# Optimization experiments

Hardware: AMD Instinct MI355X
Metric: run time of the kernel (lower is better)

The kernel has to match this reference:

```python
import jax, jax.numpy as jnp
import numpy as np

B, T, D, H, F = 4, 2048, 1024, 16, 4096
HD = D // H
EPS = 1e-5


def setup_inputs() -> dict:
    key = jax.random.key(0)
    ks = jax.random.split(key, 10)
    s = lambda fan_in: 1.0 / np.sqrt(fan_in)
    return {
        "x": jax.random.normal(ks[0], (B, T, D), jnp.float32),
        "ln1_g": jnp.ones((D,), jnp.float32),
        "ln1_b": jnp.zeros((D,), jnp.float32),
        "ln2_g": jnp.ones((D,), jnp.float32),
        "ln2_b": jnp.zeros((D,), jnp.float32),
        "Wq": jax.random.normal(ks[1], (H, D, HD), jnp.float32) * s(D),
        "Wk": jax.random.normal(ks[2], (H, D, HD), jnp.float32) * s(D),
        "Wv": jax.random.normal(ks[3], (H, D, HD), jnp.float32) * s(D),
        "Wo": jax.random.normal(ks[4], (D, D), jnp.float32) * s(D),
        "bo": jnp.zeros((D,), jnp.float32),
        "W1": jax.random.normal(ks[5], (D, F), jnp.float32) * s(D),
        "b1": jnp.zeros((F,), jnp.float32),
        "W2": jax.random.normal(ks[6], (F, D), jnp.float32) * s(F),
        "b2": jnp.zeros((D,), jnp.float32),
    }


def _layernorm(x, g, b):
    mu = jnp.mean(x, axis=-1, keepdims=True)
    var = jnp.mean(jnp.square(x - mu), axis=-1, keepdims=True)
    return (x - mu) * jax.lax.rsqrt(var + EPS) * g + b


def reference(x, ln1_g, ln1_b, ln2_g, ln2_b, Wq, Wk, Wv, Wo, bo, W1, b1, W2, b2):
    Bc, Tc, Dc = x.shape
    xn = _layernorm(x, ln1_g, ln1_b)
    # per-head projections (source loops over heads; here batched over h)
    q = jnp.einsum('btd,hdk->bhtk', xn, Wq)
    k = jnp.einsum('btd,hdk->bhtk', xn, Wk)
    v = jnp.einsum('btd,hdk->bhtk', xn, Wv)
    scale = jnp.asarray(Dc, x.dtype) ** -0.5  # C**-0.5 with C = embedding_dim
    scores = jnp.einsum('bhtk,bhsk->bhts', q, k) * scale
    causal = jnp.tril(jnp.ones((Tc, Tc), bool))
    scores = jnp.where(causal, scores, -jnp.inf)
    attn = jax.nn.softmax(scores, axis=-1)
    out = jnp.einsum('bhts,bhsk->bhtk', attn, v)
    out = out.transpose(0, 2, 1, 3).reshape(Bc, Tc, Dc)  # concat heads
    attn_out = out @ Wo + bo
    h = attn_out + x  # residual 1
    hn = _layernorm(h, ln2_g, ln2_b)
    ff = jax.nn.relu(hn @ W1 + b1) @ W2 + b2
    return ff + h  # residual 2
```

## Files before the change

### kernel.cpp

```cpp
#include <hip/hip_runtime.h>
#include <hip/hip_bf16.h>

#define NB 4
#define NT 2048
#define ND 1024
#define NH 16
#define NHD 64
#define NF 4096
#define MTOK (NB*NT)

typedef float f32x4 __attribute__((ext_vector_type(4)));
typedef __bf16 bf16x8 __attribute__((ext_vector_type(8)));
typedef short s16x8 __attribute__((ext_vector_type(8)));
typedef unsigned short ushort_t;

__device__ inline ushort_t f2bf(float f) {
    unsigned int u = __builtin_bit_cast(unsigned int, f);
    unsigned int r = (u + 0x7FFFu + ((u >> 16) & 1u)) >> 16;
    return (ushort_t)r;
}

__device__ __forceinline__ void async_load16(const void* g, void* l) {
    __builtin_amdgcn_global_load_lds(
        (const __attribute__((address_space(1))) void*)g,
        (__attribute__((address_space(3))) void*)l, 16, 0, 0);
}

__device__ __forceinline__ unsigned int cvt_pk_bf16(float lo, float hi) {
    unsigned int r;
    asm("v_cvt_pk_bf16_f32 %0, %1, %2" : "=v"(r) : "v"(lo), "v"(hi));
    return r;
}

__device__ __forceinline__ float exp2_fast(float x) {
    float r;
    asm("v_exp_f32 %0, %1" : "=v"(r) : "v"(x));
    return r;
}

__global__ __launch_bounds__(256)
void transpose_to_bf16(const float* __restrict__ src, ushort_t* __restrict__ dst,
                       int R, int C) {
    __shared__ float tile[32][33];
    int c0 = blockIdx.x * 32, r0 = blockIdx.y * 32;
    #pragma unroll
    for (int i = 0; i < 32; i += 8)
        tile[threadIdx.y + i][threadIdx.x] =
            src[(size_t)(r0 + threadIdx.y + i) * C + c0 + threadIdx.x];
    __syncthreads();
    #pragma unroll
    for (int i = 0; i < 32; i += 8)
        dst[(size_t)(c0 + threadIdx.y + i) * R + r0 + threadIdx.x] =
            f2bf(tile[threadIdx.x][threadIdx.y + i]);
}

__global__ __launch_bounds__(256)
void transpose_qkv_to_bf16(const float* __restrict__ Wq, const float* __restrict__ Wk,
                           const float* __restrict__ Wv, ushort_t* __restrict__ dst) {
    __shared__ float tile[32][33];
    int z = blockIdx.z;
    int w = z >> 4, h = z & 15;
    const float* src = (w == 0 ? Wq : (w == 1 ? Wk : Wv)) + (size_t)h * ND * NHD;
    const float sc = (w == 0) ? 0.03125f * 1.44269504f : 1.0f;
    ushort_t* out = dst + ((size_t)w * ND + h * NHD) * ND;
    int c0 = blockIdx.x * 32, r0 = blockIdx.y * 32;
    #pragma unroll
    for (int i = 0; i < 32; i += 8)
        tile[threadIdx.y + i][threadIdx.x] =
            src[(size_t)(r0 + threadIdx.y + i) * NHD + c0 + threadIdx.x];
    __syncthreads();
    #pragma unroll
    for (int i = 0; i < 32; i += 8)
        out[(size_t)(c0 + threadIdx.y + i) * ND + r0 + threadIdx.x] =
            f2bf(tile[threadIdx.x][threadIdx.y + i] * sc);
}

__global__ __launch_bounds__(256)
void layernorm_to_bf16(const float* __restrict__ x, const float* __restrict__ g,
                       const float* __restrict__ bvec, ushort_t* __restrict__ out) {
    int row = blockIdx.x;
    const float4* xr = (const float4*)(x + (size_t)row * ND);
    float4 v = xr[threadIdx.x];
    float s = v.x + v.y + v.z + v.w;
    float s2 = v.x * v.x + v.y * v.y + v.z * v.z + v.w * v.w;
    #pragma unroll
    for (int o = 32; o >= 1; o >>= 1) {
        s += __shfl_xor(s, o);
        s2 += __shfl_xor(s2, o);
    }
    __shared__ float red[8];
    int wave = threadIdx.x >> 6, lane = threadIdx.x & 63;
    if (lane == 0) { red[wave] = s; red[4 + wave] = s2; }
    __syncthreads();
    float ts = red[0] + red[1] + red[2] + red[3];
    float ts2 = red[4] + red[5] + red[6] + red[7];
    float mu = ts * (1.f / ND);
    float var = ts2 * (1.f / ND) - mu * mu;
    float rs = rsqrtf(var + 1e-5f);
    float4 gv = ((const float4*)g)[threadIdx.x];
    float4 bv = ((const float4*)bvec)[threadIdx.x];
    ushort4 o4;
    o4.x = f2bf((v.x - mu) * rs * gv.x + bv.x);
    o4.y = f2bf((v.y - mu) * rs * gv.y + bv.y);
    o4.z = f2bf((v.z - mu) * rs * gv.z + bv.z);
    o4.w = f2bf((v.w - mu) * rs * gv.w + bv.w);
    ((ushort4*)(out + (size_t)row * ND))[threadIdx.x] = o4;
}

template<int BN, bool HAS_BIAS, bool RELU, bool HAS_RES, bool OUT_F32>
__global__ __launch_bounds__(512, 2)
void gemm256(const ushort_t* __restrict__ A, const ushort_t* __restrict__ Bt,
             const float* __restrict__ bias, const float* __restrict__ res,
             void* __restrict__ outp, int M, int N, int K) {
    constexpr int NFR = BN / 64;
    constexpr int BISS = BN / 64;
    __shared__ __align__(16) ushort_t As[2][256 * 64];
    __shared__ __align__(16) ushort_t Bs[2][BN * 64];
    const int t = threadIdx.x;
    const int wave = t >> 6, lane = t & 63;
    const int wm = wave >> 2, wn = wave & 3;
    const int g = lane >> 4, l16 = lane & 15;
    int wid = blockIdx.y * gridDim.x + blockIdx.x;
    const int cpx = (gridDim.x * gridDim.y) >> 3;
    wid = (wid & 7) * cpx + (wid >> 3);
    const int m0 = (wid / gridDim.x) * 256;
    const int n0 = (wid % gridDim.x) * BN;
    const int lrow8 = lane >> 3;
    const int srcCol = ((lane & 7) ^ lrow8) * 8;
    const ushort_t* Abase = A + (size_t)m0 * K + srcCol;
    const ushort_t* Bbase = Bt + (size_t)n0 * K + srcCol;
    const int NKT = K >> 6;

    f32x4 acc[8][NFR] = {};

    auto stageA = [&](int kt, int slot) {
        #pragma unroll
        for (int j = 0; j < 4; j++) {
            const int rowbase = j * 64 + wave * 8;
            async_load16(Abase + (size_t)(rowbase + lrow8) * K + kt * 64,
                         &As[slot][rowbase * 64]);
        }
    };
    auto stageB = [&](int kt, int slot) {
        #pragma unroll
        for (int j = 0; j < BISS; j++) {
            const int rowbase = j * 64 + wave * 8;
            async_load16(Bbase + (size_t)(rowbase + lrow8) * K + kt * 64,
                         &Bs[slot][rowbase * 64]);
        }
    };

    stageA(0, 0);
    stageB(0, 0);
    stageB(1, 1);

    for (int kt = 0; kt < NKT; ++kt) {
        const int cur = kt & 1;
        if (kt == NKT - 1) {
            asm volatile("s_waitcnt vmcnt(0)" ::: "memory");
        } else if constexpr (BN == 256) {
            asm volatile("s_waitcnt vmcnt(4)" ::: "memory");
        } else {
            asm volatile("s_waitcnt vmcnt(2)" ::: "memory");
        }
        __builtin_amdgcn_s_barrier();

        const ushort_t* as = As[cur];
        const ushort_t* bs = Bs[cur];

        bf16x8 bfr[NFR][2];
        #pragma unroll
        for (int nf = 0; nf < NFR; nf++)
            #pragma unroll
            for (int ks = 0; ks < 2; ks++) {
                const int row = wn * (BN / 4) + nf * 16 + l16;
                int a = row * 128 + ks * 64 + 16 * g;
                a ^= (row & 7) << 4;
                bfr[nf][ks] = *(const bf16x8*)((const char*)bs + a);
            }
        if (kt + 1 < NKT) stageA(kt + 1, cur ^ 1);

        #pragma unroll
        for (int q = 0; q < 4; q++) {
            if (q == 2) {
                __builtin_amdgcn_s_barrier();
                if (kt + 2 < NKT) stageB(kt + 2, cur);
            }
            bf16x8 af[2][2];
            #pragma unroll
            for (int mi2 = 0; mi2 < 2; mi2++)
                #pragma unroll
                for (int ks = 0; ks < 2; ks++) {
                    const int row = wm * 128 + (q * 2 + mi2) * 16 + l16;
                    int a = row * 128 + ks * 64 + 16 * g;
                    a ^= (row & 7) << 4;
                    af[mi2][ks] = *(const bf16x8*)((const char*)as + a);
                }
            __builtin_amdgcn_s_setprio(1);
            #pragma unroll
            for (int mi2 = 0; mi2 < 2; mi2++)
                #pragma unroll
                for (int nf = 0; nf < NFR; nf++)
                    #pragma unroll
                    for (int ks = 0; ks < 2; ks++)
                        acc[q * 2 + mi2][nf] = __builtin_amdgcn_mfma_f32_16x16x32_bf16(
                            af[mi2][ks], bfr[nf][ks], acc[q * 2 + mi2][nf], 0, 0, 0);
            __builtin_amdgcn_s_setprio(0);
        }
    }

    const int gr0 = m0 + wm * 128 + g * 4;
    const int gc0 = n0 + wn * (BN / 4) + l16;
    #pragma unroll
    for (int mi = 0; mi < 8; mi++) {
        #pragma unroll
        for (int nf = 0; nf < NFR; nf++) {
            const int col = gc0 + nf * 16;
            float bb = 0.f;
            if constexpr (HAS_BIAS) bb = bias[col];
            #pragma unroll
            for (int r = 0; r < 4; r++) {
                const int row = gr0 + mi * 16 + r;
                float v = acc[mi][nf][r] + bb;
                if constexpr (RELU) v = fmaxf(v, 0.f);
                if constexpr (HAS_RES) v += res[(size_t)row * N + col];
                if constexpr (OUT_F32)
                    ((float*)outp)[(size_t)row * N + col] = v;
                else
                    ((ushort_t*)outp)[(size_t)row * N + col] = f2bf(v);
            }
        }
    }
}

__global__ __launch_bounds__(256)
void attn_kernel(const ushort_t* __restrict__ qkv, ushort_t* __restrict__ out) {
    __shared__ __align__(16) ushort_t Ks[64 * 64];
    __shared__ __align__(16) ushort_t Vt[64 * 64];
    __shared__ unsigned int Pw[4][32][35];
    const int L = blockIdx.y * gridDim.x + blockIdx.x;
    const int xcd = L & 7, kk = L >> 3;
    const int bh = ((kk & 7) << 3) | xcd;
    const int pairIdx = kk >> 3;
    const int b = bh >> 4, h = bh & 15;
    const int t = threadIdx.x, wave = t >> 6, lane = t & 63;
    const int g = lane >> 4, q16 = lane & 15;
    const size_t base = ((size_t)b * NT) * 3072 + h * NHD;
    const ushort_t* qp_base = qkv + base;
    const ushort_t* kb = qkv + base + 1024;
    const ushort_t* vb = qkv + base + 2048;
    const int krw = lane >> 3, kck = lane & 7;
    const int ksrc = (kck ^ krw) * 8;
    const int vkp = t >> 3, vdg = t & 7;

    for (int half = 0; half < 2; half++) {
        const int qt = half ? (15 - pairIdx) : pairIdx;
        const int q0 = qt * 128;
        const int wq0 = q0 + wave * 32;
        bf16x8 qf[2][2];
        #pragma unroll
        for (int qb2 = 0; qb2 < 2; qb2++) {
            const ushort_t* qp = qp_base + (size_t)(wq0 + 16 * qb2 + q16) * 3072 + 8 * g;
            qf[qb2][0] = *(const bf16x8*)qp;
            qf[qb2][1] = *(const bf16x8*)(qp + 32);
        }
        f32x4 of[2][4] = {};
        float m_run[2] = {-1.0e30f, -1.0e30f};
        float l_run[2] = {0.f, 0.f};
        const int nkv = 2 * qt + 2;

        for (int kv = 0; kv < nkv; ++kv) {
            __syncthreads();
            #pragma unroll
            for (int c = 0; c < 2; c++) {
                const int rowbase = c * 32 + wave * 8;
                async_load16(kb + (size_t)(kv * 64 + rowbase + krw) * 3072 + ksrc,
                             Ks + rowbase * 64);
            }
            {
                const ushort_t* vp = vb + (size_t)(kv * 64 + 2 * vkp) * 3072 + vdg * 8;
                s16x8 v0 = *(const s16x8*)vp;
                s16x8 v1 = *(const s16x8*)(vp + 3072);
                #pragma unroll
                for (int dd = 0; dd < 8; dd++) {
                    int d = vdg * 8 + dd;
                    unsigned int wv = (unsigned int)(ushort_t)v0[dd] |
                                      ((unsigned int)(ushort_t)v1[dd] << 16);
                    int a = (d << 7) + (vkp << 2);
                    a ^= (((d & 7) ^ ((d >> 3) & 7)) << 4);
                    *(unsigned int*)((char*)Vt + a) = wv;
                }
            }
            __syncthreads();

            const int kbase = kv * 64;
            if (kbase > wq0 + 31) continue;

            bf16x8 kf[4][2];
            #pragma unroll
            for (int n = 0; n < 4; n++)
                #pragma unroll
                for (int kd = 0; kd < 2; kd++) {
                    int row = n * 16 + q16;
                    int a = row * 128 + (kd * 64 + 16 * g);
                    a ^= ((row & 7) << 4);
                    kf[n][kd] = *(const bf16x8*)((const char*)Ks + a);
                }

            f32x4 sf[2][4] = {};
            #pragma unroll
            for (int n = 0; n < 4; n++)
                #pragma unroll
                for (int kd = 0; kd < 2; kd++) {
                    sf[0][n] = __builtin_amdgcn_mfma_f32_16x16x32_bf16(
                        kf[n][kd], qf[0][kd], sf[0][n], 0, 0, 0);
                    sf[1][n] = __builtin_amdgcn_mfma_f32_16x16x32_bf16(
                        kf[n][kd], qf[1][kd], sf[1][n], 0, 0, 0);
                }

            #pragma unroll
            for (int qb2 = 0; qb2 < 2; qb2++) {
                const int wqb = wq0 + 16 * qb2 + q16;
                const bool partial = (kbase + 63 > wq0 + 16 * qb2);
                float p[4][4];
                #pragma unroll
                for (int n = 0; n < 4; n++)
                    #pragma unroll
                    for (int r = 0; r < 4; r++) {
                        float v = sf[qb2][n][r];
                        if (partial) {
                            int kg = kbase + n * 16 + 4 * g + r;
                            if (kg > wqb) v = -1.0e30f;
                        }
                        p[n][r] = v;
                    }
                float mx0 = fmaxf(fmaxf(p[0][0], p[0][1]), fmaxf(p[0][2], p[0][3]));
                float mx1 = fmaxf(fmaxf(p[1][0], p[1][1]), fmaxf(p[1][2], p[1][3]));
                float mx2 = fmaxf(fmaxf(p[2][0], p[2][1]), fmaxf(p[2][2], p[2][3]));
                float mx3 = fmaxf(fmaxf(p[3][0], p[3][1]), fmaxf(p[3][2], p[3][3]));
                float mx = fmaxf(fmaxf(mx0, mx1), fmaxf(mx2, mx3));
                mx = fmaxf(mx, __shfl_xor(mx, 16));
                mx = fmaxf(mx, __shfl_xor(mx, 32));
                if (__any(mx > m_run[qb2] + 11.5f)) {
                    float mn = fmaxf(m_run[qb2], mx);
                    float corr = exp2_fast(m_run[qb2] - mn);
                    m_run[qb2] = mn;
                    l_run[qb2] *= corr;
                    #pragma unroll
                    for (int nf = 0; nf < 4; nf++) {
                        f32x4 o4 = of[qb2][nf];
                        o4[0] *= corr; o4[1] *= corr; o4[2] *= corr; o4[3] *= corr;
                        of[qb2][nf] = o4;
                    }
                }
                float ps = 0.f;
                #pragma unroll
                for (int n = 0; n < 4; n++)
                    #pragma unroll
                    for (int r = 0; r < 4; r++) {
                        p[n][r] = exp2_fast(p[n][r] - m_run[qb2]);
                        ps += p[n][r];
                    }
                ps += __shfl_xor(ps, 16);
                ps += __shfl_xor(ps, 32);
                l_run[qb2] += ps;
                unsigned int* pr = &Pw[wave][16 * qb2 + q16][0];
                #pragma unroll
                for (int n = 0; n < 4; n++) {
                    pr[8 * n + 2 * g + 0] = cvt_pk_bf16(p[n][0], p[n][1]);
                    pr[8 * n + 2 * g + 1] = cvt_pk_bf16(p[n][2], p[n][3]);
                }
            }

            #pragma unroll
            for (int kbk = 0; kbk < 2; kbk++) {
                bf16x8 pfr[2];
                #pragma unroll
                for (int qb2 = 0; qb2 < 2; qb2++) {
                    const unsigned int* pr = &Pw[wave][16 * qb2 + q16][0];
                    uint4 pu;
                    pu.x = pr[16 * kbk + 4 * g + 0];
                    pu.y = pr[16 * kbk + 4 * g + 1];
                    pu.z = pr[16 * kbk + 4 * g + 2];
                    pu.w = pr[16 * kbk + 4 * g + 3];
                    pfr[qb2] = __builtin_bit_cast(bf16x8, pu);
                }
                #pragma unroll
                for (int nf = 0; nf < 4; nf++) {
                    const int d = nf * 16 + q16;
                    int a = (d << 7) + (kbk * 64 + 16 * g);
                    a ^= (((d & 7) ^ ((d >> 3) & 7)) << 4);
                    bf16x8 vf = *(const bf16x8*)((const char*)Vt + a);
                    of[0][nf] = __builtin_amdgcn_mfma_f32_16x16x32_bf16(
                        vf, pfr[0], of[0][nf], 0, 0, 0);
                    of[1][nf] = __builtin_amdgcn_mfma_f32_16x16x32_bf16(
                        vf, pfr[1], of[1][nf], 0, 0, 0);
                }
            }
        }

        #pragma unroll
        for (int qb2 = 0; qb2 < 2; qb2++) {
            float rl = 1.f / l_run[qb2];
            const size_t orow = (size_t)b * NT + q0 + wave * 32 + 16 * qb2 + q16;
            #pragma unroll
            for (int nf = 0; nf < 4; nf++) {
                ushort4 o4;
                o4.x = f2bf(of[qb2][nf][0] * rl);
                o4.y = f2bf(of[qb2][nf][1] * rl);
                o4.z = f2bf(of[qb2][nf][2] * rl);
                o4.w = f2bf(of[qb2][nf][3] * rl);
                *(ushort4*)(out + orow * ND + h * NHD + nf * 16 + 4 * g) = o4;
            }
        }
    }
}

extern "C" void kernel_launch(void* const* d_in, const int* in_sizes, int n_in,
                              void* d_out, int out_size, void* d_ws, size_t ws_size,
                              hipStream_t stream) {
    const float* x     = (const float*)d_in[0];
    const float* ln1_g = (const float*)d_in[1];
    const float* ln1_b = (const float*)d_in[2];
    const float* ln2_g = (const float*)d_in[3];
    const float* ln2_b = (const float*)d_in[4];
    const float* Wq    = (const float*)d_in[5];
    const float* Wk    = (const float*)d_in[6];
    const float* Wv    = (const float*)d_in[7];
    const float* Wo    = (const float*)d_in[8];
    const float* bo    = (const float*)d_in[9];
    const float* W1    = (const float*)d_in[10];
    const float* b1    = (const float*)d_in[11];
    const float* W2    = (const float*)d_in[12];
    const float* b2    = (const float*)d_in[13];
    float* outp = (float*)d_out;

    char* w = (char*)d_ws;
    ushort_t* Wqkv_t = (ushort_t*)(w);
    ushort_t* Wo_t   = (ushort_t*)(w + 6291456);
    ushort_t* W1_t   = (ushort_t*)(w + 8388608);
    ushort_t* W2_t   = (ushort_t*)(w + 16777216);
    ushort_t* xn     = (ushort_t*)(w + 25165824);
    ushort_t* qkv    = (ushort_t*)(w + 41943040);
    ushort_t* attn_o = qkv + (size_t)MTOK * 3072;
    ushort_t* ff1    = qkv;
    float*    hbuf   = (float*)(w + 41943040 + 67108864);

    dim3 tb(32, 8);
    transpose_qkv_to_bf16<<<dim3(2, 32, 48), tb, 0, stream>>>(Wq, Wk, Wv, Wqkv_t);
    transpose_to_bf16<<<dim3(32, 32), tb, 0, stream>>>(Wo, Wo_t, 1024, 1024);
    transpose_to_bf16<<<dim3(128, 32), tb, 0, stream>>>(W1, W1_t, 1024, 4096);
    transpose_to_bf16<<<dim3(32, 128), tb, 0, stream>>>(W2, W2_t, 4096, 1024);

    layernorm_to_bf16<<<MTOK, 256, 0, stream>>>(x, ln1_g, ln1_b, xn);

    gemm256<128, false, false, false, false><<<dim3(24, 32), 512, 0, stream>>>(
        xn, Wqkv_t, nullptr, nullptr, qkv, MTOK, 3072, 1024);

    attn_kernel<<<dim3(8, 64), 256, 0, stream>>>(qkv, attn_o);

    gemm256<128, true, false, true, true><<<dim3(8, 32), 512, 0, stream>>>(
        attn_o, Wo_t, bo, x, hbuf, MTOK, 1024, 1024);

    layernorm_to_bf16<<<MTOK, 256, 0, stream>>>(hbuf, ln2_g, ln2_b, xn);

    gemm256<256, true, true, false, false><<<dim3(16, 32), 512, 0, stream>>>(
        xn, W1_t, b1, nullptr, ff1, MTOK, NF, 1024);

    gemm256<128, true, false, true, true><<<dim3(8, 32), 512, 0, stream>>>(
        ff1, W2_t, b2, hbuf, outp, MTOK, 1024, NF);
}
```

Before: 388.9 us.

## Restructure GEMM into 8-phase half-tile load pipeline with per-phase barriers

Rewrites the bf16 GEMM main loop so that A and B tile loads are issued in halves spread across four compute phases per k-step. Each phase has its own vmcnt wait and barriers, and the wave-to-row mapping of A fragments is interleaved so every phase reads a 64-row slice written by one half-load. The aim is to overlap global-to-LDS traffic with MFMA work more evenly and avoid one large wait at the top of each iteration. In exchange it adds more barriers per iteration and relies on tight vmcnt accounting, where a mistake would cause races.

```diff
diff --git a/kernel.cpp b/kernel.cpp
--- a/kernel.cpp
+++ b/kernel.cpp
@@ -109,11 +109,10 @@
 
 template<int BN, bool HAS_BIAS, bool RELU, bool HAS_RES, bool OUT_F32>
 __global__ __launch_bounds__(512, 2)
-void gemm256(const ushort_t* __restrict__ A, const ushort_t* __restrict__ Bt,
-             const float* __restrict__ bias, const float* __restrict__ res,
-             void* __restrict__ outp, int M, int N, int K) {
+void gemm8p(const ushort_t* __restrict__ A, const ushort_t* __restrict__ Bt,
+            const float* __restrict__ bias, const float* __restrict__ res,
+            void* __restrict__ outp, int M, int N, int K) {
     constexpr int NFR = BN / 64;
-    constexpr int BISS = BN / 64;
     __shared__ __align__(16) ushort_t As[2][256 * 64];
     __shared__ __align__(16) ushort_t Bs[2][BN * 64];
     const int t = threadIdx.x;
@@ -133,69 +132,79 @@
 
     f32x4 acc[8][NFR] = {};
 
-    auto stageA = [&](int kt, int slot) {
+    auto stageAhalf = [&](int kt, int h, int slot) {
         #pragma unroll
-        for (int j = 0; j < 4; j++) {
+        for (int j = 2 * h; j < 2 * h + 2; j++) {
             const int rowbase = j * 64 + wave * 8;
             async_load16(Abase + (size_t)(rowbase + lrow8) * K + kt * 64,
                          &As[slot][rowbase * 64]);
         }
     };
-    auto stageB = [&](int kt, int slot) {
-        #pragma unroll
-        for (int j = 0; j < BISS; j++) {
-            const int rowbase = j * 64 + wave * 8;
+    auto stageBhalf = [&](int kt, int h, int slot) {
+        if constexpr (BN == 256) {
+            #pragma unroll
+            for (int j = 2 * h; j < 2 * h + 2; j++) {
+                const int rowbase = j * 64 + wave * 8;
+                async_load16(Bbase + (size_t)(rowbase + lrow8) * K + kt * 64,
+                             &Bs[slot][rowbase * 64]);
+            }
+        } else {
+            const int rowbase = h * 64 + wave * 8;
             async_load16(Bbase + (size_t)(rowbase + lrow8) * K + kt * 64,
                          &Bs[slot][rowbase * 64]);
         }
     };
 
-    stageA(0, 0);
-    stageB(0, 0);
-    stageB(1, 1);
+    stageAhalf(0, 0, 0); stageAhalf(0, 1, 0);
+    stageBhalf(0, 0, 0); stageBhalf(0, 1, 0);
+    stageBhalf(1, 0, 1); stageBhalf(1, 1, 1);
+    stageAhalf(1, 0, 1);
+    if constexpr (BN == 256) asm volatile("s_waitcnt vmcnt(6)" ::: "memory");
+    else                     asm volatile("s_waitcnt vmcnt(4)" ::: "memory");
+    __builtin_amdgcn_s_barrier();
+    __builtin_amdgcn_sched_barrier(0);
 
     for (int kt = 0; kt < NKT; ++kt) {
-        const int cur = kt & 1;
-        if (kt == NKT - 1) {
-            asm volatile("s_waitcnt vmcnt(0)" ::: "memory");
-        } else if constexpr (BN == 256) {
-            asm volatile("s_waitcnt vmcnt(4)" ::: "memory");
-        } else {
-            asm volatile("s_waitcnt vmcnt(2)" ::: "memory");
-        }
-        __builtin_amdgcn_s_barrier();
-
+        const int cur = kt & 1, nxt = cur ^ 1;
         const ushort_t* as = As[cur];
         const ushort_t* bs = Bs[cur];
-
         bf16x8 bfr[NFR][2];
         #pragma unroll
-        for (int nf = 0; nf < NFR; nf++)
-            #pragma unroll
-            for (int ks = 0; ks < 2; ks++) {
-                const int row = wn * (BN / 4) + nf * 16 + l16;
-                int a = row * 128 + ks * 64 + 16 * g;
-                a ^= (row & 7) << 4;
-                bfr[nf][ks] = *(const bf16x8*)((const char*)bs + a);
-            }
-        if (kt + 1 < NKT) stageA(kt + 1, cur ^ 1);
-
-        #pragma unroll
         for (int q = 0; q < 4; q++) {
-            if (q == 2) {
-                __builtin_amdgcn_s_barrier();
-                if (kt + 2 < NKT) stageB(kt + 2, cur);
+            if (q == 0) {
+                #pragma unroll
+                for (int nf = 0; nf < NFR; nf++)
+                    #pragma unroll
+                    for (int ks = 0; ks < 2; ks++) {
+                        const int row = wn * (BN / 4) + nf * 16 + l16;
+                        int a = row * 128 + ks * 64 + 16 * g;
+                        a ^= (row & 7) << 4;
+                        bfr[nf][ks] = *(const bf16x8*)((const char*)bs + a);
+                    }
             }
             bf16x8 af[2][2];
             #pragma unroll
             for (int mi2 = 0; mi2 < 2; mi2++)
                 #pragma unroll
                 for (int ks = 0; ks < 2; ks++) {
-                    const int row = wm * 128 + (q * 2 + mi2) * 16 + l16;
+                    const int row = q * 64 + wm * 32 + mi2 * 16 + l16;
                     int a = row * 128 + ks * 64 + 16 * g;
                     a ^= (row & 7) << 4;
                     af[mi2][ks] = *(const bf16x8*)((const char*)as + a);
                 }
+            if (q == 0)      { if (kt + 1 < NKT) stageAhalf(kt + 1, 1, nxt); }
+            else if (q == 1) { if (kt + 2 < NKT) stageBhalf(kt + 2, 0, cur); }
+            else if (q == 2) { if (kt + 2 < NKT) stageBhalf(kt + 2, 1, cur); }
+            else             { if (kt + 2 < NKT) stageAhalf(kt + 2, 0, cur); }
+            __builtin_amdgcn_sched_barrier(0);
+            if (kt < NKT - 2) {
+                if constexpr (BN == 256) asm volatile("s_waitcnt vmcnt(8)" ::: "memory");
+                else                     asm volatile("s_waitcnt vmcnt(6)" ::: "memory");
+            } else {
+                asm volatile("s_waitcnt vmcnt(0)" ::: "memory");
+            }
+            __builtin_amdgcn_s_barrier();
+            __builtin_amdgcn_sched_barrier(0);
             __builtin_amdgcn_s_setprio(1);
             #pragma unroll
             for (int mi2 = 0; mi2 < 2; mi2++)
@@ -206,13 +215,15 @@
                         acc[q * 2 + mi2][nf] = __builtin_amdgcn_mfma_f32_16x16x32_bf16(
                             af[mi2][ks], bfr[nf][ks], acc[q * 2 + mi2][nf], 0, 0, 0);
             __builtin_amdgcn_s_setprio(0);
+            __builtin_amdgcn_s_barrier();
+            __builtin_amdgcn_sched_barrier(0);
         }
     }
 
-    const int gr0 = m0 + wm * 128 + g * 4;
     const int gc0 = n0 + wn * (BN / 4) + l16;
     #pragma unroll
     for (int mi = 0; mi < 8; mi++) {
+        const int rowb = m0 + (mi >> 1) * 64 + wm * 32 + (mi & 1) * 16 + g * 4;
         #pragma unroll
         for (int nf = 0; nf < NFR; nf++) {
             const int col = gc0 + nf * 16;
@@ -220,7 +231,7 @@
             if constexpr (HAS_BIAS) bb = bias[col];
             #pragma unroll
             for (int r = 0; r < 4; r++) {
-                const int row = gr0 + mi * 16 + r;
+                const int row = rowb + r;
                 float v = acc[mi][nf][r] + bb;
                 if constexpr (RELU) v = fmaxf(v, 0.f);
                 if constexpr (HAS_RES) v += res[(size_t)row * N + col];
@@ -454,19 +465,19 @@
 
     layernorm_to_bf16<<<MTOK, 256, 0, stream>>>(x, ln1_g, ln1_b, xn);
 
-    gemm256<128, false, false, false, false><<<dim3(24, 32), 512, 0, stream>>>(
+    gemm8p<128, false, false, false, false><<<dim3(24, 32), 512, 0, stream>>>(
         xn, Wqkv_t, nullptr, nullptr, qkv, MTOK, 3072, 1024);
 
     attn_kernel<<<dim3(8, 64), 256, 0, stream>>>(qkv, attn_o);
 
-    gemm256<128, true, false, true, true><<<dim3(8, 32), 512, 0, stream>>>(
+    gemm8p<128, true, false, true, true><<<dim3(8, 32), 512, 0, stream>>>(
         attn_o, Wo_t, bo, x, hbuf, MTOK, 1024, 1024);
 
     layernorm_to_bf16<<<MTOK, 256, 0, stream>>>(hbuf, ln2_g, ln2_b, xn);
 
-    gemm256<256, true, true, false, false><<<dim3(16, 32), 512, 0, stream>>>(
+    gemm8p<256, true, true, false, false><<<dim3(16, 32), 512, 0, stream>>>(
         xn, W1_t, b1, nullptr, ff1, MTOK, NF, 1024);
 
-    gemm256<128, true, false, true, true><<<dim3(8, 32), 512, 0, stream>>>(
+    gemm8p<128, true, false, true, true><<<dim3(8, 32), 512, 0, stream>>>(
         ff1, W2_t, b2, hbuf, outp, MTOK, 1024, NF);
 }
```

Result: slower. 396.8 us (+2.0%).

## Double-buffer K/V tiles in attention kernel to overlap loads with compute

Applied to the files above, without the earlier changes.

The attention kernel now keeps two LDS buffers each for K and transposed V. It issues the global loads for the next KV tile before computing on the current one, then writes V into the other buffer after compute, leaving one barrier per iteration. This is meant to hide global-load latency behind the MFMA and softmax work. It doubles K/V LDS use, which may lower occupancy, and raises register pressure because the prefetched V values are held across the compute.

```diff
diff --git a/kernel.cpp b/kernel.cpp
--- a/kernel.cpp
+++ b/kernel.cpp
@@ -235,8 +235,8 @@
 
 __global__ __launch_bounds__(256)
 void attn_kernel(const ushort_t* __restrict__ qkv, ushort_t* __restrict__ out) {
-    __shared__ __align__(16) ushort_t Ks[64 * 64];
-    __shared__ __align__(16) ushort_t Vt[64 * 64];
+    __shared__ __align__(16) ushort_t Ks[2][64 * 64];
+    __shared__ __align__(16) ushort_t Vt[2][64 * 64];
     __shared__ unsigned int Pw[4][32][35];
     const int L = blockIdx.y * gridDim.x + blockIdx.x;
     const int xcd = L & 7, kk = L >> 3;
@@ -253,6 +253,31 @@
     const int ksrc = (kck ^ krw) * 8;
     const int vkp = t >> 3, vdg = t & 7;
 
+    auto stageK = [&](int kv, int buf) {
+        #pragma unroll
+        for (int c = 0; c < 2; c++) {
+            const int rowbase = c * 32 + wave * 8;
+            async_load16(kb + (size_t)(kv * 64 + rowbase + krw) * 3072 + ksrc,
+                         &Ks[buf][rowbase * 64]);
+        }
+    };
+    auto loadV = [&](int kv, s16x8& v0, s16x8& v1) {
+        const ushort_t* vp = vb + (size_t)(kv * 64 + 2 * vkp) * 3072 + vdg * 8;
+        v0 = *(const s16x8*)vp;
+        v1 = *(const s16x8*)(vp + 3072);
+    };
+    auto writeV = [&](int buf, const s16x8& v0, const s16x8& v1) {
+        #pragma unroll
+        for (int dd = 0; dd < 8; dd++) {
+            int d = vdg * 8 + dd;
+            unsigned int wv = (unsigned int)(ushort_t)v0[dd] |
+                              ((unsigned int)(ushort_t)v1[dd] << 16);
+            int a = (d << 7) + (vkp << 2);
+            a ^= (((d & 7) ^ ((d >> 3) & 7)) << 4);
+            *(unsigned int*)((char*)&Vt[buf][0] + a) = wv;
+        }
+    };
+
     for (int half = 0; half < 2; half++) {
         const int qt = half ? (15 - pairIdx) : pairIdx;
         const int q0 = qt * 128;
@@ -269,134 +294,132 @@
         float l_run[2] = {0.f, 0.f};
         const int nkv = 2 * qt + 2;
 
+        {
+            s16x8 pv0, pv1;
+            stageK(0, 0);
+            loadV(0, pv0, pv1);
+            asm volatile("s_waitcnt vmcnt(0)" ::: "memory");
+            writeV(0, pv0, pv1);
+        }
+        __syncthreads();
+
         for (int kv = 0; kv < nkv; ++kv) {
+            const int cur = kv & 1, nxt = cur ^ 1;
+            s16x8 pv0, pv1;
+            const bool pre = (kv + 1 < nkv);
+            if (pre) {
+                stageK(kv + 1, nxt);
+                loadV(kv + 1, pv0, pv1);
+            }
+            __builtin_amdgcn_sched_barrier(0);
+
+            const int kbase = kv * 64;
+            if (kbase <= wq0 + 31) {
+                bf16x8 kf[4][2];
+                #pragma unroll
+                for (int n = 0; n < 4; n++)
+                    #pragma unroll
+                    for (int kd = 0; kd < 2; kd++) {
+                        int row = n * 16 + q16;
+                        int a = row * 128 + (kd * 64 + 16 * g);
+                        a ^= ((row & 7) << 4);
+                        kf[n][kd] = *(const bf16x8*)((const char*)&Ks[cur][0] + a);
+                    }
+
+                f32x4 sf[2][4] = {};
+                #pragma unroll
+                for (int n = 0; n < 4; n++)
+                    #pragma unroll
+                    for (int kd = 0; kd < 2; kd++) {
+                        sf[0][n] = __builtin_amdgcn_mfma_f32_16x16x32_bf16(
+                            kf[n][kd], qf[0][kd], sf[0][n], 0, 0, 0);
+                        sf[1][n] = __builtin_amdgcn_mfma_f32_16x16x32_bf16(
+                            kf[n][kd], qf[1][kd], sf[1][n], 0, 0, 0);
+                    }
+
+                #pragma unroll
+                for (int qb2 = 0; qb2 < 2; qb2++) {
+                    const int wqb = wq0 + 16 * qb2 + q16;
+                    const bool partial = (kbase + 63 > wq0 + 16 * qb2);
+                    float p[4][4];
+                    #pragma unroll
+                    for (int n = 0; n < 4; n++)
+                        #pragma unroll
+                        for (int r = 0; r < 4; r++) {
+                            float v = sf[qb2][n][r];
+                            if (partial) {
+                                int kg = kbase + n * 16 + 4 * g + r;
+                                if (kg > wqb) v = -1.0e30f;
+                            }
+                            p[n][r] = v;
+                        }
+                    float mx0 = fmaxf(fmaxf(p[0][0], p[0][1]), fmaxf(p[0][2], p[0][3]));
+                    float mx1 = fmaxf(fmaxf(p[1][0], p[1][1]), fmaxf(p[1][2], p[1][3]));
+                    float mx2 = fmaxf(fmaxf(p[2][0], p[2][1]), fmaxf(p[2][2], p[2][3]));
+                    float mx3 = fmaxf(fmaxf(p[3][0], p[3][1]), fmaxf(p[3][2], p[3][3]));
+                    float mx = fmaxf(fmaxf(mx0, mx1), fmaxf(mx2, mx3));
+                    mx = fmaxf(mx, __shfl_xor(mx, 16));
+                    mx = fmaxf(mx, __shfl_xor(mx, 32));
+                    if (__any(mx > m_run[qb2] + 11.5f)) {
+                        float mn = fmaxf(m_run[qb2], mx);
+                        float corr = exp2_fast(m_run[qb2] - mn);
+                        m_run[qb2] = mn;
+                        l_run[qb2] *= corr;
+                        #pragma unroll
+                        for (int nf = 0; nf < 4; nf++) {
+                            f32x4 o4 = of[qb2][nf];
+                            o4[0] *= corr; o4[1] *= corr; o4[2] *= corr; o4[3] *= corr;
+                            of[qb2][nf] = o4;
+                        }
+                    }
+                    float ps = 0.f;
+                    #pragma unroll
+                    for (int n = 0; n < 4; n++)
+                        #pragma unroll
+                        for (int r = 0; r < 4; r++) {
+                            p[n][r] = exp2_fast(p[n][r] - m_run[qb2]);
+                            ps += p[n][r];
+                        }
+                    ps += __shfl_xor(ps, 16);
+                    ps += __shfl_xor(ps, 32);
+                    l_run[qb2] += ps;
+                    unsigned int* pr = &Pw[wave][16 * qb2 + q16][0];
+                    #pragma unroll
+                    for (int n = 0; n < 4; n++) {
+                        pr[8 * n + 2 * g + 0] = cvt_pk_bf16(p[n][0], p[n][1]);
+                        pr[8 * n + 2 * g + 1] = cvt_pk_bf16(p[n][2], p[n][3]);
+                    }
+                }
+
+                #pragma unroll
+                for (int kbk = 0; kbk < 2; kbk++) {
+                    bf16x8 pfr[2];
+                    #pragma unroll
+                    for (int qb2 = 0; qb2 < 2; qb2++) {
+                        const unsigned int* pr = &Pw[wave][16 * qb2 + q16][0];
+                        uint4 pu;
+                        pu.x = pr[16 * kbk + 4 * g + 0];
+                        pu.y = pr[16 * kbk + 4 * g + 1];
+                        pu.z = pr[16 * kbk + 4 * g + 2];
+                        pu.w = pr[16 * kbk + 4 * g + 3];
+                        pfr[qb2] = __builtin_bit_cast(bf16x8, pu);
+                    }
+                    #pragma unroll
+                    for (int nf = 0; nf < 4; nf++) {
+                        const int d = nf * 16 + q16;
+                        int a = (d << 7) + (kbk * 64 + 16 * g);
+                        a ^= (((d & 7) ^ ((d >> 3) & 7)) << 4);
+                        bf16x8 vf = *(const bf16x8*)((const char*)&Vt[cur][0] + a);
+                        of[0][nf] = __builtin_amdgcn_mfma_f32_16x16x32_bf16(
+                            vf, pfr[0], of[0][nf], 0, 0, 0);
+                        of[1][nf] = __builtin_amdgcn_mfma_f32_16x16x32_bf16(
+                            vf, pfr[1], of[1][nf], 0, 0, 0);
+                    }
+                }
+            }
+
+            if (pre) writeV(nxt, pv0, pv1);
             __syncthreads();
-            #pragma unroll
-            for (int c = 0; c < 2; c++) {
-                const int rowbase = c * 32 + wave * 8;
-                async_load16(kb + (size_t)(kv * 64 + rowbase + krw) * 3072 + ksrc,
-                             Ks + rowbase * 64);
-            }
-            {
-                const ushort_t* vp = vb + (size_t)(kv * 64 + 2 * vkp) * 3072 + vdg * 8;
-                s16x8 v0 = *(const s16x8*)vp;
-                s16x8 v1 = *(const s16x8*)(vp + 3072);
-                #pragma unroll
-                for (int dd = 0; dd < 8; dd++) {
-                    int d = vdg * 8 + dd;
-                    unsigned int wv = (unsigned int)(ushort_t)v0[dd] |
-                                      ((unsigned int)(ushort_t)v1[dd] << 16);
-                    int a = (d << 7) + (vkp << 2);
-                    a ^= (((d & 7) ^ ((d >> 3) & 7)) << 4);
-                    *(unsigned int*)((char*)Vt + a) = wv;
-                }
-            }
-            __syncthreads();
-
-            const int kbase = kv * 64;
-            if (kbase > wq0 + 31) continue;
-
-            bf16x8 kf[4][2];
-            #pragma unroll
-            for (int n = 0; n < 4; n++)
-                #pragma unroll
-                for (int kd = 0; kd < 2; kd++) {
-                    int row = n * 16 + q16;
-                    int a = row * 128 + (kd * 64 + 16 * g);
-                    a ^= ((row & 7) << 4);
-                    kf[n][kd] = *(const bf16x8*)((const char*)Ks + a);
-                }
-
-            f32x4 sf[2][4] = {};
-            #pragma unroll
-            for (int n = 0; n < 4; n++)
-                #pragma unroll
-                for (int kd = 0; kd < 2; kd++) {
-                    sf[0][n] = __builtin_amdgcn_mfma_f32_16x16x32_bf16(
-                        kf[n][kd], qf[0][kd], sf[0][n], 0, 0, 0);
-                    sf[1][n] = __builtin_amdgcn_mfma_f32_16x16x32_bf16(
-                        kf[n][kd], qf[1][kd], sf[1][n], 0, 0, 0);
-                }
-
-            #pragma unroll
-            for (int qb2 = 0; qb2 < 2; qb2++) {
-                const int wqb = wq0 + 16 * qb2 + q16;
-                const bool partial = (kbase + 63 > wq0 + 16 * qb2);
-                float p[4][4];
-                #pragma unroll
-                for (int n = 0; n < 4; n++)
-                    #pragma unroll
-                    for (int r = 0; r < 4; r++) {
-                        float v = sf[qb2][n][r];
-                        if (partial) {
-                            int kg = kbase + n * 16 + 4 * g + r;
-                            if (kg > wqb) v = -1.0e30f;
-                        }
-                        p[n][r] = v;
-                    }
-                float mx0 = fmaxf(fmaxf(p[0][0], p[0][1]), fmaxf(p[0][2], p[0][3]));
-                float mx1 = fmaxf(fmaxf(p[1][0], p[1][1]), fmaxf(p[1][2], p[1][3]));
-                float mx2 = fmaxf(fmaxf(p[2][0], p[2][1]), fmaxf(p[2][2], p[2][3]));
-                float mx3 = fmaxf(fmaxf(p[3][0], p[3][1]), fmaxf(p[3][2], p[3][3]));
-                float mx = fmaxf(fmaxf(mx0, mx1), fmaxf(mx2, mx3));
-                mx = fmaxf(mx, __shfl_xor(mx, 16));
-                mx = fmaxf(mx, __shfl_xor(mx, 32));
-                if (__any(mx > m_run[qb2] + 11.5f)) {
-                    float mn = fmaxf(m_run[qb2], mx);
-                    float corr = exp2_fast(m_run[qb2] - mn);
-                    m_run[qb2] = mn;
-                    l_run[qb2] *= corr;
-                    #pragma unroll
-                    for (int nf = 0; nf < 4; nf++) {
-                        f32x4 o4 = of[qb2][nf];
-                        o4[0] *= corr; o4[1] *= corr; o4[2] *= corr; o4[3] *= corr;
-                        of[qb2][nf] = o4;
-                    }
-                }
-                float ps = 0.f;
-                #pragma unroll
-                for (int n = 0; n < 4; n++)
-                    #pragma unroll
-                    for (int r = 0; r < 4; r++) {
-                        p[n][r] = exp2_fast(p[n][r] - m_run[qb2]);
-                        ps += p[n][r];
-                    }
-                ps += __shfl_xor(ps, 16);
-                ps += __shfl_xor(ps, 32);
-                l_run[qb2] += ps;
-                unsigned int* pr = &Pw[wave][16 * qb2 + q16][0];
-                #pragma unroll
-                for (int n = 0; n < 4; n++) {
-                    pr[8 * n + 2 * g + 0] = cvt_pk_bf16(p[n][0], p[n][1]);
-                    pr[8 * n + 2 * g + 1] = cvt_pk_bf16(p[n][2], p[n][3]);
-                }
-            }
-
-            #pragma unroll
-            for (int kbk = 0; kbk < 2; kbk++) {
-                bf16x8 pfr[2];
-                #pragma unroll
-                for (int qb2 = 0; qb2 < 2; qb2++) {
-                    const unsigned int* pr = &Pw[wave][16 * qb2 + q16][0];
-                    uint4 pu;
-                    pu.x = pr[16 * kbk + 4 * g + 0];
-                    pu.y = pr[16 * kbk + 4 * g + 1];
-                    pu.z = pr[16 * kbk + 4 * g + 2];
-                    pu.w = pr[16 * kbk + 4 * g + 3];
-                    pfr[qb2] = __builtin_bit_cast(bf16x8, pu);
-                }
-                #pragma unroll
-                for (int nf = 0; nf < 4; nf++) {
-                    const int d = nf * 16 + q16;
-                    int a = (d << 7) + (kbk * 64 + 16 * g);
-                    a ^= (((d & 7) ^ ((d >> 3) & 7)) << 4);
-                    bf16x8 vf = *(const bf16x8*)((const char*)Vt + a);
-                    of[0][nf] = __builtin_amdgcn_mfma_f32_16x16x32_bf16(
-                        vf, pfr[0], of[0][nf], 0, 0, 0);
-                    of[1][nf] = __builtin_amdgcn_mfma_f32_16x16x32_bf16(
-                        vf, pfr[1], of[1][nf], 0, 0, 0);
-                }
-            }
         }
 
         #pragma unroll
```

Result: no change. 390.7 us (+0.5%).
